# Kernel tuning notes

Measured on AMD Instinct MI355X. Metric: run time of the kernel, lower is better.

## Reference

```python
import jax, jax.numpy as jnp
import numpy as np

N_NODES = 100000
N_EDGES = 1600000
IN_C, HID, OUT_C = 100, 128, 47
N_HID_LAYERS = 3  # SAGEConv(hid->hid) count; +1 final SAGEConv(hid->out)


def setup_inputs() -> dict:
    key = jax.random.key(0)
    ks = jax.random.split(key, 8)
    x = jax.random.normal(ks[0], (N_NODES, IN_C), dtype=jnp.float32)
    edge_index = jax.random.randint(ks[1], (2, N_EDGES), 0, N_NODES, dtype=jnp.int32)
    s = 0.05  # weight scale for numeric stability
    return {
        "x": x,
        "edge_index": edge_index,
        "inproj_w": jax.random.normal(ks[2], (IN_C, HID), dtype=jnp.float32) * s,
        "inproj_b": jnp.zeros((HID,), jnp.float32),
        "wl_h": jax.random.normal(ks[3], (N_HID_LAYERS, HID, HID), dtype=jnp.float32) * s,
        "bl_h": jnp.zeros((N_HID_LAYERS, HID), jnp.float32),
        "wr_h": jax.random.normal(ks[4], (N_HID_LAYERS, HID, HID), dtype=jnp.float32) * s,
        "wl_out": jax.random.normal(ks[5], (HID, OUT_C), dtype=jnp.float32) * s,
        "bl_out": jnp.zeros((OUT_C,), jnp.float32),
        "wr_out": jax.random.normal(ks[6], (HID, OUT_C), dtype=jnp.float32) * s,
    }


def reference(x, edge_index, inproj_w, inproj_b, wl_h, bl_h, wr_h, wl_out, bl_out, wr_out):
    n = x.shape[0]
    src, dst = edge_index[0], edge_index[1]
    # in-degree for mean aggregation (clamped to avoid div-by-zero)
    deg = jax.ops.segment_sum(jnp.ones_like(dst, dtype=x.dtype), dst, num_segments=n)
    deg = jnp.maximum(deg, 1.0)[:, None]

    def sage(h, wl, bl, wr):
        # mean over incoming-edge messages, then lin_l(agg) + lin_r(h)
        agg = jax.ops.segment_sum(h[src], dst, num_segments=n) / deg
        return agg @ wl + bl + h @ wr

    h = x @ inproj_w + inproj_b
    inp = h
    h = jax.nn.relu(h)
    for i in range(N_HID_LAYERS):
        h = sage(h, wl_h[i], bl_h[i], wr_h[i])
        h = jax.nn.relu(h) + 0.2 * inp  # dropout is identity in eval mode
    h = sage(h, wl_out, bl_out, wr_out)
    return jax.nn.log_softmax(h, axis=-1)
```

## Files before the change

### kernel.cpp

```cpp
#include <hip/hip_runtime.h>
#include <math.h>

#define HIDC 128
#define INC 100
#define OUTC 47

typedef __attribute__((ext_vector_type(8))) short short8_t;
typedef __attribute__((ext_vector_type(4))) float f32x4;

__device__ inline unsigned short f2bf(float f) {
    unsigned u = __builtin_bit_cast(unsigned, f);
    unsigned r = (u + 0x7FFFu + ((u >> 16) & 1u)) >> 16;
    return (unsigned short)r;
}
__device__ inline float bf2f(unsigned short s) {
    unsigned u = ((unsigned)s) << 16;
    return __builtin_bit_cast(float, u);
}


__global__ __launch_bounds__(256) void k_deg(const int* __restrict__ dst, int* __restrict__ deg, int ne) {
    int e = blockIdx.x * 256 + threadIdx.x;
    if (e < ne) atomicAdd(&deg[dst[e]], 1);
}

__global__ __launch_bounds__(256) void k_scan1(const int* __restrict__ deg, int* __restrict__ local_s,
                                               int* __restrict__ bsum, int n) {
    __shared__ int s[256];
    int t = threadIdx.x;
    int i = blockIdx.x * 256 + t;
    int v = (i < n) ? deg[i] : 0;
    s[t] = v;
    __syncthreads();
    for (int off = 1; off < 256; off <<= 1) {
        int add = (t >= off) ? s[t - off] : 0;
        __syncthreads();
        s[t] += add;
        __syncthreads();
    }
    if (i < n) local_s[i] = s[t] - v;
    if (t == 255) bsum[blockIdx.x] = s[255];
}

__global__ __launch_bounds__(512) void k_scan2(int* __restrict__ bsum, int nb) {
    __shared__ int s[512];
    int t = threadIdx.x;
    int v = (t < nb) ? bsum[t] : 0;
    s[t] = v;
    __syncthreads();
    for (int off = 1; off < 512; off <<= 1) {
        int add = (t >= off) ? s[t - off] : 0;
        __syncthreads();
        s[t] += add;
        __syncthreads();
    }
    if (t < nb) bsum[t] = s[t] - v;
}

__global__ __launch_bounds__(256) void k_scan3(const int* __restrict__ local_s, const int* __restrict__ bsum,
                                               int* __restrict__ offs, int n, int ne) {
    int i = blockIdx.x * 256 + threadIdx.x;
    if (i < n) offs[i] = local_s[i] + bsum[blockIdx.x];
    if (i == 0) offs[n] = ne;
}

__global__ __launch_bounds__(256) void k_invdeg(const int* __restrict__ deg, float* __restrict__ invdeg, int n) {
    int i = blockIdx.x * 256 + threadIdx.x;
    if (i < n) invdeg[i] = 1.0f / (float)max(deg[i], 1);
}

__global__ __launch_bounds__(256) void k_fill(const int* __restrict__ src, const int* __restrict__ dst,
                                              const int* __restrict__ offs, int* __restrict__ curs,
                                              int* __restrict__ csr, int ne) {
    int e = blockIdx.x * 256 + threadIdx.x;
    if (e < ne) {
        int d = dst[e];
        int p = atomicAdd(&curs[d], 1);
        csr[offs[d] + p] = src[e];
    }
}


__global__ __launch_bounds__(256) void k_prepw(const float* __restrict__ wl_h, const float* __restrict__ wr_h,
                                               unsigned short* __restrict__ wt) {
    int idx = blockIdx.x * 256 + threadIdx.x;
    if (idx >= 6 * 16384) return;
    int m = idx >> 14, rem = idx & 16383;
    int l = m >> 1, s = m & 1;
    const float* srcm = (s == 0 ? wl_h : wr_h) + (size_t)l * 16384;
    wt[idx] = f2bf(srcm[(rem & 127) * 128 + (rem >> 7)]);
}


__global__ __launch_bounds__(256) void k_agg(const unsigned short* __restrict__ h, const int* __restrict__ csr,
                                             const int* __restrict__ offs, const float* __restrict__ invdeg,
                                             unsigned short* __restrict__ agg, int n) {
    int wv = threadIdx.x >> 6, lane = threadIdx.x & 63;
    int v = blockIdx.x * 4 + wv;
    if (v >= n) return;
    int q = lane >> 4, c = lane & 15;
    int e0 = offs[v], e1 = offs[v + 1];
    float acc[8] = {0, 0, 0, 0, 0, 0, 0, 0};
    for (int e = e0 + q; e < e1; e += 4) {
        int sidx = csr[e];
        short8_t tv = *reinterpret_cast<const short8_t*>(h + (size_t)sidx * HIDC + c * 8);
#pragma unroll
        for (int i = 0; i < 8; i++) acc[i] += bf2f((unsigned short)tv[i]);
    }
#pragma unroll
    for (int i = 0; i < 8; i++) {
        acc[i] += __shfl_xor(acc[i], 16);
        acc[i] += __shfl_xor(acc[i], 32);
    }
    if (q == 0) {
        float s = invdeg[v];
        unsigned short o[8];
#pragma unroll
        for (int i = 0; i < 8; i++) o[i] = f2bf(acc[i] * s);
        *reinterpret_cast<short8_t*>(agg + (size_t)v * HIDC + c * 8) = *reinterpret_cast<const short8_t*>(o);
    }
}


__global__ __launch_bounds__(256) void k_inproj(const float* __restrict__ x, const float* __restrict__ w,
                                                const float* __restrict__ b, float* __restrict__ inp,
                                                unsigned short* __restrict__ h, int n) {
    __shared__ float sX[16][INC];
    int t = threadIdx.x;
    int brow = blockIdx.x * 16;
    for (int idx = t; idx < 16 * INC; idx += 256) {
        int r = idx / INC, c = idx % INC;
        int row = brow + r;
        sX[r][c] = (row < n) ? x[(size_t)row * INC + c] : 0.f;
    }
    __syncthreads();
    int q = t >> 6, j = t & 63;
    float acc0[4] = {0, 0, 0, 0}, acc1[4] = {0, 0, 0, 0};
#pragma unroll 2
    for (int k0 = 0; k0 < INC; k0 += 4) {
        float a_[4][4];
#pragma unroll
        for (int r = 0; r < 4; r++) {
            float4 t4 = *reinterpret_cast<const float4*>(&sX[q * 4 + r][k0]);
            a_[r][0] = t4.x; a_[r][1] = t4.y; a_[r][2] = t4.z; a_[r][3] = t4.w;
        }
#pragma unroll
        for (int kk = 0; kk < 4; kk++) {
            int k = k0 + kk;
            float w0 = w[k * HIDC + j];
            float w1 = w[k * HIDC + j + 64];
#pragma unroll
            for (int r = 0; r < 4; r++) {
                acc0[r] += a_[r][kk] * w0;
                acc1[r] += a_[r][kk] * w1;
            }
        }
    }
    float b0 = b[j], b1 = b[j + 64];
#pragma unroll
    for (int r = 0; r < 4; r++) {
        int row = brow + q * 4 + r;
        if (row < n) {
            float v0 = acc0[r] + b0, v1 = acc1[r] + b1;
            inp[(size_t)row * HIDC + j] = v0;
            inp[(size_t)row * HIDC + j + 64] = v1;
            h[(size_t)row * HIDC + j] = f2bf(fmaxf(v0, 0.f));
            h[(size_t)row * HIDC + j + 64] = f2bf(fmaxf(v1, 0.f));
        }
    }
}


__global__ __launch_bounds__(256) void k_sage_mfma(const unsigned short* __restrict__ agg,
                                                   unsigned short* __restrict__ h,
                                                   const float* __restrict__ inp,
                                                   const unsigned short* __restrict__ wt,
                                                   const float* __restrict__ bl, int n) {
    __shared__ unsigned short sA[2][32 * 128];
    int t = threadIdx.x;
    int w = t >> 6, lane = t & 63;
    int cc = lane & 15, kg = lane >> 4;
    int row0 = blockIdx.x * 32;

    short8_t bfrag[2][2][4];
#pragma unroll
    for (int s = 0; s < 2; s++)
#pragma unroll
        for (int ci = 0; ci < 2; ci++) {
            int ncol = 32 * w + ci * 16 + cc;
            const unsigned short* bp = wt + s * 16384 + ncol * 128 + kg * 8;
#pragma unroll
            for (int ks = 0; ks < 4; ks++)
                bfrag[s][ci][ks] = *reinterpret_cast<const short8_t*>(bp + ks * 32);
        }

    for (int c = t; c < 512; c += 256) {
        int r = c >> 4, g = c & 15;
        int row = row0 + r;
        unsigned byte = r * 256 + (((unsigned)g * 16) ^ (((unsigned)r & 7) << 4));
        short8_t va = {0, 0, 0, 0, 0, 0, 0, 0}, vh = va;
        if (row < n) {
            va = *reinterpret_cast<const short8_t*>(agg + (size_t)row * HIDC + g * 8);
            vh = *reinterpret_cast<const short8_t*>(h + (size_t)row * HIDC + g * 8);
        }
        *reinterpret_cast<short8_t*>(reinterpret_cast<char*>(&sA[0][0]) + byte) = va;
        *reinterpret_cast<short8_t*>(reinterpret_cast<char*>(&sA[1][0]) + byte) = vh;
    }
    __syncthreads();

    f32x4 acc[2][2];
#pragma unroll
    for (int rt = 0; rt < 2; rt++)
#pragma unroll
        for (int ci = 0; ci < 2; ci++) acc[rt][ci] = (f32x4){0.f, 0.f, 0.f, 0.f};

#pragma unroll
    for (int ks = 0; ks < 4; ks++) {
        short8_t af[2][2];
#pragma unroll
        for (int s = 0; s < 2; s++)
#pragma unroll
            for (int rt = 0; rt < 2; rt++) {
                int r = rt * 16 + cc;
                unsigned byte = r * 256 + (((unsigned)(ks * 64 + kg * 16)) ^ (((unsigned)r & 7) << 4));
                af[s][rt] = *reinterpret_cast<const short8_t*>(reinterpret_cast<const char*>(&sA[s][0]) + byte);
            }
#pragma unroll
        for (int s = 0; s < 2; s++)
#pragma unroll
            for (int rt = 0; rt < 2; rt++)
#pragma unroll
                for (int ci = 0; ci < 2; ci++)
                    acc[rt][ci] = __builtin_amdgcn_mfma_f32_16x16x32_bf16(af[s][rt], bfrag[s][ci][ks],
                                                                          acc[rt][ci], 0, 0, 0);
    }

#pragma unroll
    for (int rt = 0; rt < 2; rt++)
#pragma unroll
        for (int ci = 0; ci < 2; ci++) {
            int col = 32 * w + ci * 16 + cc;
            float bv = bl[col];
#pragma unroll
            for (int reg = 0; reg < 4; reg++) {
                int row = row0 + rt * 16 + kg * 4 + reg;
                if (row < n) {
                    float v = acc[rt][ci][reg] + bv;
                    v = fmaxf(v, 0.f) + 0.2f * inp[(size_t)row * HIDC + col];
                    h[(size_t)row * HIDC + col] = f2bf(v);
                }
            }
        }
}


__global__ __launch_bounds__(256) void k_out(const unsigned short* __restrict__ agg,
                                             const unsigned short* __restrict__ h,
                                             const float* __restrict__ wl, const float* __restrict__ bl,
                                             const float* __restrict__ wr, float* __restrict__ out, int n) {
    __shared__ float sA[16][HIDC];
    __shared__ float sH[16][HIDC];
    __shared__ float sO[16][48];
    int t = threadIdx.x;
    int brow = blockIdx.x * 16;
    for (int idx = t; idx < 256; idx += 256) {
        int r = idx >> 4, g = idx & 15;
        int row = brow + r;
        short8_t va = {0, 0, 0, 0, 0, 0, 0, 0}, vh = va;
        if (row < n) {
            va = *reinterpret_cast<const short8_t*>(agg + (size_t)row * HIDC + g * 8);
            vh = *reinterpret_cast<const short8_t*>(h + (size_t)row * HIDC + g * 8);
        }
#pragma unroll
        for (int i = 0; i < 8; i++) {
            sA[r][g * 8 + i] = bf2f((unsigned short)va[i]);
            sH[r][g * 8 + i] = bf2f((unsigned short)vh[i]);
        }
    }
    __syncthreads();
    int q = t >> 6, j = t & 63;
    if (j < OUTC) {
        float acc[4] = {0, 0, 0, 0};
#pragma unroll 2
        for (int k0 = 0; k0 < HIDC; k0 += 4) {
            float a_[4][4], h_[4][4];
#pragma unroll
            for (int r = 0; r < 4; r++) {
                float4 t4 = *reinterpret_cast<const float4*>(&sA[q * 4 + r][k0]);
                a_[r][0] = t4.x; a_[r][1] = t4.y; a_[r][2] = t4.z; a_[r][3] = t4.w;
                float4 t5 = *reinterpret_cast<const float4*>(&sH[q * 4 + r][k0]);
                h_[r][0] = t5.x; h_[r][1] = t5.y; h_[r][2] = t5.z; h_[r][3] = t5.w;
            }
#pragma unroll
            for (int kk = 0; kk < 4; kk++) {
                int k = k0 + kk;
                float wlv = wl[k * OUTC + j];
                float wrv = wr[k * OUTC + j];
#pragma unroll
                for (int r = 0; r < 4; r++) acc[r] += a_[r][kk] * wlv + h_[r][kk] * wrv;
            }
        }
        float bv = bl[j];
#pragma unroll
        for (int r = 0; r < 4; r++) sO[q * 4 + r][j] = acc[r] + bv;
    }
    __syncthreads();
    int lane = t & 63;
#pragma unroll
    for (int r = 0; r < 4; r++) {
        int row = brow + q * 4 + r;
        bool act = (lane < OUTC) && (row < n);
        float val = act ? sO[q * 4 + r][lane] : -INFINITY;
        float m = val;
#pragma unroll
        for (int off = 32; off; off >>= 1) m = fmaxf(m, __shfl_xor(m, off));
        float ex = act ? __expf(val - m) : 0.f;
        float s = ex;
#pragma unroll
        for (int off = 32; off; off >>= 1) s += __shfl_xor(s, off);
        if (act) out[(size_t)row * OUTC + lane] = val - m - logf(s);
    }
}


extern "C" void kernel_launch(void* const* d_in, const int* in_sizes, int n_in,
                              void* d_out, int out_size, void* d_ws, size_t ws_size,
                              hipStream_t stream) {
    const float* x        = (const float*)d_in[0];
    const int*   ei       = (const int*)d_in[1];
    const float* inproj_w = (const float*)d_in[2];
    const float* inproj_b = (const float*)d_in[3];
    const float* wl_h     = (const float*)d_in[4];
    const float* bl_h     = (const float*)d_in[5];
    const float* wr_h     = (const float*)d_in[6];
    const float* wl_out   = (const float*)d_in[7];
    const float* bl_out   = (const float*)d_in[8];
    const float* wr_out   = (const float*)d_in[9];
    float* out = (float*)d_out;

    int n  = in_sizes[0] / INC;
    int ne = in_sizes[1] / 2;
    const int* src = ei;
    const int* dst = ei + ne;

    char* ws = (char*)d_ws;
    size_t off = 0;
    auto alloc = [&](size_t bytes) -> void* {
        void* p = ws + off;
        off = (off + bytes + 255) & ~(size_t)255;
        return p;
    };
    float*          inp    = (float*)alloc((size_t)n * HIDC * 4);
    unsigned short* h      = (unsigned short*)alloc((size_t)n * HIDC * 2);
    unsigned short* agg    = (unsigned short*)alloc((size_t)n * HIDC * 2);
    unsigned short* wt     = (unsigned short*)alloc((size_t)6 * 16384 * 2);
    int*   deg    = (int*)alloc((size_t)n * 4);
    float* invdeg = (float*)alloc((size_t)n * 4);
    int*   local_s= (int*)alloc((size_t)n * 4);
    int*   bsum   = (int*)alloc(512 * 4);
    int*   offs   = (int*)alloc((size_t)(n + 1) * 4);
    int*   curs   = (int*)alloc((size_t)n * 4);
    int*   csr    = (int*)alloc((size_t)ne * 4);

    hipMemsetAsync(deg, 0, (size_t)n * 4, stream);
    hipMemsetAsync(curs, 0, (size_t)n * 4, stream);

    int nbE = (ne + 255) / 256;
    int nbN = (n + 255) / 256;
    k_deg<<<nbE, 256, 0, stream>>>(dst, deg, ne);
    k_scan1<<<nbN, 256, 0, stream>>>(deg, local_s, bsum, n);
    k_scan2<<<1, 512, 0, stream>>>(bsum, nbN);
    k_scan3<<<nbN, 256, 0, stream>>>(local_s, bsum, offs, n, ne);
    k_invdeg<<<nbN, 256, 0, stream>>>(deg, invdeg, n);
    k_fill<<<nbE, 256, 0, stream>>>(src, dst, offs, curs, csr, ne);
    k_prepw<<<(6 * 16384 + 255) / 256, 256, 0, stream>>>(wl_h, wr_h, wt);

    int nbR = (n + 15) / 16;
    int nbA = (n + 3) / 4;
    int nbT = (n + 31) / 32;
    k_inproj<<<nbR, 256, 0, stream>>>(x, inproj_w, inproj_b, inp, h, n);
    for (int l = 0; l < 3; ++l) {
        k_agg<<<nbA, 256, 0, stream>>>(h, csr, offs, invdeg, agg, n);
        k_sage_mfma<<<nbT, 256, 0, stream>>>(agg, h, inp, wt + (size_t)l * 2 * 16384,
                                             bl_h + (size_t)l * HIDC, n);
    }
    k_agg<<<nbA, 256, 0, stream>>>(h, csr, offs, invdeg, agg, n);
    k_out<<<nbR, 256, 0, stream>>>(agg, h, wl_out, bl_out, wr_out, out, n);
}
```

Before: 737.8 us.

## Use MFMA bf16 for output SAGE layer and unroll edge gather by two

Replaces the scalar fp32 output layer kernel with an MFMA bf16 kernel. Weights are pre-transposed and zero-padded to 48 columns, LDS tiles are XOR-swizzled, and log-softmax is done with 16-lane shuffles. Separately, the aggregation loop now loads two neighbor rows per iteration so more memory loads are in flight. This trades fp32 precision in the final matmul for bf16 and adds a small weight-prep kernel.

```diff
diff --git a/kernel.cpp b/kernel.cpp
--- a/kernel.cpp
+++ b/kernel.cpp
@@ -91,6 +91,17 @@
     wt[idx] = f2bf(srcm[(rem & 127) * 128 + (rem >> 7)]);
 }
 
+__global__ __launch_bounds__(256) void k_prepw_out(const float* __restrict__ wl_out,
+                                                   const float* __restrict__ wr_out,
+                                                   unsigned short* __restrict__ wt2) {
+    int idx = blockIdx.x * 256 + threadIdx.x;
+    if (idx >= 2 * 48 * 128) return;
+    int s = idx / (48 * 128), rem = idx % (48 * 128);
+    int nc = rem >> 7, k = rem & 127;
+    const float* srcm = (s == 0) ? wl_out : wr_out;
+    wt2[idx] = (nc < OUTC) ? f2bf(srcm[k * OUTC + nc]) : 0;
+}
+
 
 __global__ __launch_bounds__(256) void k_agg(const unsigned short* __restrict__ h, const int* __restrict__ csr,
                                              const int* __restrict__ offs, const float* __restrict__ invdeg,
@@ -101,11 +112,17 @@
     int q = lane >> 4, c = lane & 15;
     int e0 = offs[v], e1 = offs[v + 1];
     float acc[8] = {0, 0, 0, 0, 0, 0, 0, 0};
-    for (int e = e0 + q; e < e1; e += 4) {
-        int sidx = csr[e];
-        short8_t tv = *reinterpret_cast<const short8_t*>(h + (size_t)sidx * HIDC + c * 8);
-#pragma unroll
-        for (int i = 0; i < 8; i++) acc[i] += bf2f((unsigned short)tv[i]);
+    for (int e = e0 + q; e < e1; e += 8) {
+        int s0 = csr[e];
+        bool has2 = (e + 4) < e1;
+        int s1 = has2 ? csr[e + 4] : s0;
+        short8_t t0 = *reinterpret_cast<const short8_t*>(h + (size_t)s0 * HIDC + c * 8);
+        short8_t t1 = *reinterpret_cast<const short8_t*>(h + (size_t)s1 * HIDC + c * 8);
+#pragma unroll
+        for (int i = 0; i < 8; i++) {
+            acc[i] += bf2f((unsigned short)t0[i]);
+            if (has2) acc[i] += bf2f((unsigned short)t1[i]);
+        }
     }
 #pragma unroll
     for (int i = 0; i < 8; i++) {
@@ -254,71 +271,90 @@
 }
 
 
-__global__ __launch_bounds__(256) void k_out(const unsigned short* __restrict__ agg,
-                                             const unsigned short* __restrict__ h,
-                                             const float* __restrict__ wl, const float* __restrict__ bl,
-                                             const float* __restrict__ wr, float* __restrict__ out, int n) {
-    __shared__ float sA[16][HIDC];
-    __shared__ float sH[16][HIDC];
-    __shared__ float sO[16][48];
+__global__ __launch_bounds__(256) void k_out_mfma(const unsigned short* __restrict__ agg,
+                                                  const unsigned short* __restrict__ h,
+                                                  const unsigned short* __restrict__ wt2,
+                                                  const float* __restrict__ bl,
+                                                  float* __restrict__ out, int n) {
+    __shared__ unsigned short sA[2][64 * 128];
     int t = threadIdx.x;
-    int brow = blockIdx.x * 16;
-    for (int idx = t; idx < 256; idx += 256) {
-        int r = idx >> 4, g = idx & 15;
-        int row = brow + r;
+    int w = t >> 6, lane = t & 63;
+    int cc = lane & 15, kg = lane >> 4;
+    int row0 = blockIdx.x * 64;
+
+    short8_t bfrag[2][3][4];
+#pragma unroll
+    for (int s = 0; s < 2; s++)
+#pragma unroll
+        for (int ci = 0; ci < 3; ci++) {
+            const unsigned short* bp = wt2 + s * (48 * 128) + (ci * 16 + cc) * 128 + kg * 8;
+#pragma unroll
+            for (int ks = 0; ks < 4; ks++)
+                bfrag[s][ci][ks] = *reinterpret_cast<const short8_t*>(bp + ks * 32);
+        }
+
+    for (int c = t; c < 1024; c += 256) {
+        int r = c >> 4, g = c & 15;
+        int row = row0 + r;
+        unsigned byte = r * 256 + (((unsigned)g * 16) ^ (((unsigned)r & 7) << 4));
         short8_t va = {0, 0, 0, 0, 0, 0, 0, 0}, vh = va;
         if (row < n) {
             va = *reinterpret_cast<const short8_t*>(agg + (size_t)row * HIDC + g * 8);
             vh = *reinterpret_cast<const short8_t*>(h + (size_t)row * HIDC + g * 8);
         }
-#pragma unroll
-        for (int i = 0; i < 8; i++) {
-            sA[r][g * 8 + i] = bf2f((unsigned short)va[i]);
-            sH[r][g * 8 + i] = bf2f((unsigned short)vh[i]);
-        }
+        *reinterpret_cast<short8_t*>(reinterpret_cast<char*>(&sA[0][0]) + byte) = va;
+        *reinterpret_cast<short8_t*>(reinterpret_cast<char*>(&sA[1][0]) + byte) = vh;
     }
     __syncthreads();
-    int q = t >> 6, j = t & 63;
-    if (j < OUTC) {
-        float acc[4] = {0, 0, 0, 0};
-#pragma unroll 2
-        for (int k0 = 0; k0 < HIDC; k0 += 4) {
-            float a_[4][4], h_[4][4];
-#pragma unroll
-            for (int r = 0; r < 4; r++) {
-                float4 t4 = *reinterpret_cast<const float4*>(&sA[q * 4 + r][k0]);
-                a_[r][0] = t4.x; a_[r][1] = t4.y; a_[r][2] = t4.z; a_[r][3] = t4.w;
-                float4 t5 = *reinterpret_cast<const float4*>(&sH[q * 4 + r][k0]);
-                h_[r][0] = t5.x; h_[r][1] = t5.y; h_[r][2] = t5.z; h_[r][3] = t5.w;
+
+    f32x4 acc[3];
+#pragma unroll
+    for (int ci = 0; ci < 3; ci++) acc[ci] = (f32x4){0.f, 0.f, 0.f, 0.f};
+
+#pragma unroll
+    for (int ks = 0; ks < 4; ks++) {
+        short8_t af[2];
+        int r = w * 16 + cc;
+        unsigned byte = r * 256 + (((unsigned)(ks * 64 + kg * 16)) ^ (((unsigned)r & 7) << 4));
+#pragma unroll
+        for (int s = 0; s < 2; s++)
+            af[s] = *reinterpret_cast<const short8_t*>(reinterpret_cast<const char*>(&sA[s][0]) + byte);
+#pragma unroll
+        for (int s = 0; s < 2; s++)
+#pragma unroll
+            for (int ci = 0; ci < 3; ci++)
+                acc[ci] = __builtin_amdgcn_mfma_f32_16x16x32_bf16(af[s], bfrag[s][ci][ks], acc[ci], 0, 0, 0);
+    }
+
+#pragma unroll
+    for (int reg = 0; reg < 4; reg++) {
+        int row = row0 + w * 16 + kg * 4 + reg;
+        float val[3];
+        float m = -INFINITY;
+#pragma unroll
+        for (int ci = 0; ci < 3; ci++) {
+            int col = ci * 16 + cc;
+            val[ci] = (col < OUTC) ? (acc[ci][reg] + bl[col]) : -INFINITY;
+            m = fmaxf(m, val[ci]);
+        }
+#pragma unroll
+        for (int off = 1; off < 16; off <<= 1) m = fmaxf(m, __shfl_xor(m, off));
+        float s = 0.f;
+#pragma unroll
+        for (int ci = 0; ci < 3; ci++) {
+            int col = ci * 16 + cc;
+            if (col < OUTC) s += __expf(val[ci] - m);
+        }
+#pragma unroll
+        for (int off = 1; off < 16; off <<= 1) s += __shfl_xor(s, off);
+        float lse = m + logf(s);
+        if (row < n) {
+#pragma unroll
+            for (int ci = 0; ci < 3; ci++) {
+                int col = ci * 16 + cc;
+                if (col < OUTC) out[(size_t)row * OUTC + col] = val[ci] - lse;
             }
-#pragma unroll
-            for (int kk = 0; kk < 4; kk++) {
-                int k = k0 + kk;
-                float wlv = wl[k * OUTC + j];
-                float wrv = wr[k * OUTC + j];
-#pragma unroll
-                for (int r = 0; r < 4; r++) acc[r] += a_[r][kk] * wlv + h_[r][kk] * wrv;
-            }
-        }
-        float bv = bl[j];
-#pragma unroll
-        for (int r = 0; r < 4; r++) sO[q * 4 + r][j] = acc[r] + bv;
-    }
-    __syncthreads();
-    int lane = t & 63;
-#pragma unroll
-    for (int r = 0; r < 4; r++) {
-        int row = brow + q * 4 + r;
-        bool act = (lane < OUTC) && (row < n);
-        float val = act ? sO[q * 4 + r][lane] : -INFINITY;
-        float m = val;
-#pragma unroll
-        for (int off = 32; off; off >>= 1) m = fmaxf(m, __shfl_xor(m, off));
-        float ex = act ? __expf(val - m) : 0.f;
-        float s = ex;
-#pragma unroll
-        for (int off = 32; off; off >>= 1) s += __shfl_xor(s, off);
-        if (act) out[(size_t)row * OUTC + lane] = val - m - logf(s);
+        }
     }
 }
 
@@ -354,6 +390,7 @@
     unsigned short* h      = (unsigned short*)alloc((size_t)n * HIDC * 2);
     unsigned short* agg    = (unsigned short*)alloc((size_t)n * HIDC * 2);
     unsigned short* wt     = (unsigned short*)alloc((size_t)6 * 16384 * 2);
+    unsigned short* wt2    = (unsigned short*)alloc((size_t)2 * 48 * 128 * 2);
     int*   deg    = (int*)alloc((size_t)n * 4);
     float* invdeg = (float*)alloc((size_t)n * 4);
     int*   local_s= (int*)alloc((size_t)n * 4);
@@ -374,10 +411,12 @@
     k_invdeg<<<nbN, 256, 0, stream>>>(deg, invdeg, n);
     k_fill<<<nbE, 256, 0, stream>>>(src, dst, offs, curs, csr, ne);
     k_prepw<<<(6 * 16384 + 255) / 256, 256, 0, stream>>>(wl_h, wr_h, wt);
+    k_prepw_out<<<(2 * 48 * 128 + 255) / 256, 256, 0, stream>>>(wl_out, wr_out, wt2);
 
     int nbR = (n + 15) / 16;
     int nbA = (n + 3) / 4;
     int nbT = (n + 31) / 32;
+    int nbO = (n + 63) / 64;
     k_inproj<<<nbR, 256, 0, stream>>>(x, inproj_w, inproj_b, inp, h, n);
     for (int l = 0; l < 3; ++l) {
         k_agg<<<nbA, 256, 0, stream>>>(h, csr, offs, invdeg, agg, n);
@@ -385,5 +424,5 @@
                                              bl_h + (size_t)l * HIDC, n);
     }
     k_agg<<<nbA, 256, 0, stream>>>(h, csr, offs, invdeg, agg, n);
-    k_out<<<nbR, 256, 0, stream>>>(agg, h, wl_out, bl_out, wr_out, out, n);
-}
+    k_out_mfma<<<nbO, 256, 0, stream>>>(agg, h, wt2, bl_out, out, n);
+}
```

Result: faster. 642.3 us (-12.9%).
